# Kernel optimization log

Hardware: AMD Instinct MI355X
Metric: run time of the kernel (lower is better)

## Reference

```python
import jax, jax.numpy as jnp
import numpy as np

NUM_GROUPS = 32
EPS = 1e-6


def group_norm(x, gamma, beta):
    # x: [b, c, t, h, w]
    b, c, t, h, w = x.shape
    xg = x.reshape(b, NUM_GROUPS, c // NUM_GROUPS, t, h, w)
    mean = xg.mean(axis=(2, 3, 4, 5), keepdims=True)
    var = xg.var(axis=(2, 3, 4, 5), keepdims=True)
    xg = (xg - mean) * jax.lax.rsqrt(var + EPS)
    xn = xg.reshape(b, c, t, h, w)
    return xn * gamma[None, :, None, None, None] + beta[None, :, None, None, None]


def conv1x1(x, w, bias):
    # 1x1x1 Conv3d == per-position channel matmul. x: [b,c,t,h,w], w: [cout,cin]
    y = jnp.einsum('oc,bcthw->bothw', w, x)
    return y + bias[None, :, None, None, None]


def setup_inputs() -> dict:
    key = jax.random.key(0)
    ks = jax.random.split(key, 11)
    c = 512
    b, t, h, w = 1, 16, 32, 32
    s = 1.0 / np.sqrt(c)
    return {
        'x': jax.random.normal(ks[0], (b, c, t, h, w), dtype=jnp.float32),
        'gn_gamma': jnp.ones((c,), jnp.float32),
        'gn_beta': jnp.zeros((c,), jnp.float32),
        'wq': jax.random.normal(ks[1], (c, c), jnp.float32) * s,
        'bq': jnp.zeros((c,), jnp.float32),
        'wk': jax.random.normal(ks[2], (c, c), jnp.float32) * s,
        'bk': jnp.zeros((c,), jnp.float32),
        'wv': jax.random.normal(ks[3], (c, c), jnp.float32) * s,
        'bv': jnp.zeros((c,), jnp.float32),
        'wo': jax.random.normal(ks[4], (c, c), jnp.float32) * s,
        'bo': jnp.zeros((c,), jnp.float32),
    }


def reference(x, gn_gamma, gn_beta, wq, bq, wk, bk, wv, bv, wo, bo):
    b, c, t, h, w = x.shape
    h_ = group_norm(x, gn_gamma, gn_beta)
    q = conv1x1(h_, wq, bq)
    k = conv1x1(h_, wk, bk)
    v = conv1x1(h_, wv, bv)
    # per-frame spatial attention: tokens are the h*w grid, batched over (b t)
    n = h * w
    q = q.transpose(0, 2, 3, 4, 1).reshape(b * t, n, c)   # [(bt), n, c]
    k = k.transpose(0, 2, 3, 4, 1).reshape(b * t, n, c)
    v = v.transpose(0, 2, 3, 4, 1).reshape(b * t, n, c)
    scale = float(int(c) ** (-0.5))
    attn = jax.nn.softmax(jnp.einsum('bic,bjc->bij', q, k) * scale, axis=-1)
    out = jnp.einsum('bij,bjc->bic', attn, v)             # [(bt), n, c]
    out = out.reshape(b, t, h, w, c).transpose(0, 4, 1, 2, 3)
    out = conv1x1(out, wo, bo)
    return x + out
```

## Files before the change

### kernel.cpp

```cpp
#include <hip/hip_runtime.h>
#include <hip/hip_bf16.h>

#define CCH   512
#define NPOS  16384
#define NTOK  1024
#define NFRM  16
#define NGRP  32
#define GSZ   (CCH / NGRP)
#define GELEM (GSZ * NPOS)
#define GN_SPLIT 32

typedef unsigned short u16;
typedef unsigned int   u32;
typedef __attribute__((ext_vector_type(8))) short  short8;
typedef __attribute__((ext_vector_type(4))) float  floatx4;

__device__ __forceinline__ float bf2f(u16 u) {
    return __uint_as_float(((u32)u) << 16);
}
__device__ __forceinline__ u16 f2bf(float f) {
    u32 u = __float_as_uint(f);
    u = (u + 0x7fffu + ((u >> 16) & 1u)) >> 16;
    return (u16)u;
}
__device__ __forceinline__ float ldx(const void* p, size_t i, bool f32m) {
    return f32m ? ((const float*)p)[i] : bf2f(((const u16*)p)[i]);
}
__device__ __forceinline__ void gl2lds16(const u16* g, u16* l) {
    __builtin_amdgcn_global_load_lds(
        (const __attribute__((address_space(1))) u32*)g,
        (__attribute__((address_space(3))) u32*)l, 16, 0, 0);
}

__launch_bounds__(256)
__global__ void detect_dtype(const u32* __restrict__ x32, u32* __restrict__ flag) {
    __shared__ int cnt;
    if (threadIdx.x == 0) cnt = 0;
    __syncthreads();
    int c = 0;
    for (int i = threadIdx.x; i < 4096; i += 256) {
        u32 v = x32[i] & 0xFFFFu;
        u32 e = (v >> 7) & 0xFFu;
        if (e >= 0xC8u) c++;
    }
    atomicAdd(&cnt, c);
    __syncthreads();
    if (threadIdx.x == 0) *flag = (cnt > 64) ? 1u : 0u;
}

__launch_bounds__(256)
__global__ void conv_all(const void* w0, const void* w1, const void* w2, const void* w3,
                         const void* b0, const void* b1, const void* b2, const void* b3,
                         u16* __restrict__ wdst, u16* __restrict__ bdst,
                         float* __restrict__ rl,
                         const u32* __restrict__ flag) {
    int b = blockIdx.x;
    if (b > 1024) {
        rl[(b - 1025) * 256 + threadIdx.x] = 0.0f;
        return;
    }
    bool f32m = *flag != 0u;
    if (b < 1024) {
        int wi = b >> 8;
        const void* src = (wi == 0) ? w0 : (wi == 1) ? w1 : (wi == 2) ? w2 : w3;
        int base = (b & 255) * 1024 + threadIdx.x * 4;
        u16* d = wdst + wi * 262144 + base;
        if (f32m) {
            float4 v = *(const float4*)((const float*)src + base);
            ushort4 o;
            o.x = f2bf(v.x); o.y = f2bf(v.y); o.z = f2bf(v.z); o.w = f2bf(v.w);
            *(ushort4*)d = o;
        } else {
            *(ushort4*)d = *(const ushort4*)((const u16*)src + base);
        }
    } else {
        int t = threadIdx.x;
        int bi = t >> 6;
        int off = (t & 63) * 8;
        const void* src = (bi == 0) ? b0 : (bi == 1) ? b1 : (bi == 2) ? b2 : b3;
        u16* d = bdst + bi * 512 + off;
        if (f32m) {
            float4 v1 = *(const float4*)((const float*)src + off);
            float4 v2 = *(const float4*)((const float*)src + off + 4);
            ushort4 o1, o2;
            o1.x = f2bf(v1.x); o1.y = f2bf(v1.y); o1.z = f2bf(v1.z); o1.w = f2bf(v1.w);
            o2.x = f2bf(v2.x); o2.y = f2bf(v2.y); o2.z = f2bf(v2.z); o2.w = f2bf(v2.w);
            *(ushort4*)d = o1; *(ushort4*)(d + 4) = o2;
        } else {
            *(ushort4*)d = *(const ushort4*)((const u16*)src + off);
            *(ushort4*)(d + 4) = *(const ushort4*)((const u16*)src + off + 4);
        }
    }
}

__launch_bounds__(256)
__global__ void gn_partial(const void* __restrict__ x, float2* __restrict__ partials,
                           const u32* __restrict__ flag) {
    __shared__ float sm[8];
    bool f32m = *flag != 0u;
    const int chunk = GELEM / GN_SPLIT;
    size_t base = (size_t)blockIdx.x * chunk;
    float s = 0.f, ss = 0.f;
    if (f32m) {
        const float4* p = (const float4*)((const float*)x + base);
        for (int i = threadIdx.x; i < chunk / 4; i += 256) {
            float4 u = p[i];
            s  += u.x + u.y + u.z + u.w;
            ss += u.x * u.x + u.y * u.y + u.z * u.z + u.w * u.w;
        }
    } else {
        const ushort4* p = (const ushort4*)((const u16*)x + base);
        for (int i = threadIdx.x; i < chunk / 4; i += 256) {
            ushort4 u = p[i];
            float a = bf2f(u.x), b = bf2f(u.y), c = bf2f(u.z), d = bf2f(u.w);
            s  += a + b + c + d;
            ss += a * a + b * b + c * c + d * d;
        }
    }
    int lane = threadIdx.x & 63, w = threadIdx.x >> 6;
    float t = s;
    #pragma unroll
    for (int o = 32; o > 0; o >>= 1) t += __shfl_down(t, o, 64);
    if (lane == 0) sm[w] = t;
    t = ss;
    #pragma unroll
    for (int o = 32; o > 0; o >>= 1) t += __shfl_down(t, o, 64);
    if (lane == 0) sm[4 + w] = t;
    __syncthreads();
    if (threadIdx.x == 0)
        partials[blockIdx.x] = make_float2(sm[0] + sm[1] + sm[2] + sm[3],
                                           sm[4] + sm[5] + sm[6] + sm[7]);
}

__launch_bounds__(256)
__global__ void gn_coef(const float2* __restrict__ partials, const void* __restrict__ gamma,
                        const void* __restrict__ beta, float2* __restrict__ coef,
                        const u32* __restrict__ flag) {
    bool f32m = *flag != 0u;
    int c = blockIdx.x * 256 + threadIdx.x;
    if (c < CCH) {
        int g = c >> 4;
        float sum = 0.f, sq = 0.f;
        #pragma unroll
        for (int i = 0; i < GN_SPLIT; ++i) {
            float2 p = partials[g * GN_SPLIT + i];
            sum += p.x; sq += p.y;
        }
        float mean = sum * (1.0f / (float)GELEM);
        float var  = fmaxf(sq * (1.0f / (float)GELEM) - mean * mean, 0.0f);
        float rstd = rsqrtf(var + 1e-6f);
        float gm = ldx(gamma, c, f32m), b = ldx(beta, c, f32m);
        float sc = rstd * gm;
        coef[c] = make_float2(sc, b - mean * sc);
    }
}

__launch_bounds__(256)
__global__ void gn_apply_t(const void* __restrict__ x, const float2* __restrict__ coef,
                           u16* __restrict__ xt, const u32* __restrict__ flag) {
    bool f32m = *flag != 0u;
    __shared__ float tile[64][65];
    int p0 = blockIdx.x * 64, c0 = blockIdx.y * 64;
    int lane = threadIdx.x & 63, rg = threadIdx.x >> 6;
    #pragma unroll 4
    for (int i = 0; i < 16; ++i) {
        int row = rg * 16 + i;
        int c = c0 + row;
        float2 cf = coef[c];
        float v = ldx(x, (size_t)c * NPOS + p0 + lane, f32m);
        tile[row][lane] = v * cf.x + cf.y;
    }
    __syncthreads();
    #pragma unroll 4
    for (int i = 0; i < 16; ++i) {
        int prow = rg * 16 + i;
        xt[(size_t)(p0 + prow) * CCH + c0 + lane] = f2bf(tile[lane][prow]);
    }
}

#define EPI_QK    0
#define EPI_V     1
#define EPI_SCEXP 2
#define EPI_PV    3
#define EPI_OUT   4

template<int EPI, bool MX, bool FSW>
__launch_bounds__(256, 3)
__global__ void mfma_gemm(const u16* __restrict__ A, const u16* __restrict__ B,
                          void* __restrict__ C, const u16* __restrict__ bias,
                          const void* __restrict__ resid, const u32* __restrict__ flag,
                          float* __restrict__ rl,
                          int lda, int ldb, int ldc, int K,
                          long aFS, long bFS, long cFS) {
    __shared__ __align__(16) u16 As[128 * 64];
    __shared__ __align__(16) u16 Bs[128 * 64];
    const int tid = threadIdx.x;

    int bxi, byi, f;
    if (FSW) {
        u32 id = (blockIdx.z * gridDim.y + blockIdx.y) * gridDim.x + blockIdx.x;
        u32 T = gridDim.x * gridDim.y * gridDim.z;
        u32 half = T >> 1;
        f = (int)(id & 7u) + ((id >= half) ? 8 : 0);
        u32 l = (id >= half ? id - half : id) >> 3;
        bxi = (int)(l % gridDim.x);
        byi = (int)(l / gridDim.x);
    } else {
        bxi = blockIdx.x; byi = blockIdx.y; f = blockIdx.z;
    }
    const int m_blk = MX ? bxi : byi;
    const int n_blk = MX ? byi : bxi;

    const u16* Ab = A + (size_t)f * aFS + (size_t)m_blk * 128 * lda;
    const u16* Bb = B + (size_t)f * bFS + (size_t)n_blk * 128 * ldb;

    const int wave = tid >> 6, lane = tid & 63;
    const int srow8 = wave * 32 + (lane >> 3);
    const int schs  = ((lane & 7) ^ ((lane >> 3) & 7)) * 8;
    u16* lA = &As[wave * 2048];
    u16* lB = &Bs[wave * 2048];

    const int wm = (wave >> 1) * 64, wn = (wave & 1) * 64;
    const int l15 = lane & 15, quad = lane >> 4;

    floatx4 acc[4][4] = {};

    for (int kk = 0; kk < K; kk += 64) {
        __syncthreads();
        #pragma unroll
        for (int o = 0; o < 4; ++o) {
            gl2lds16(Ab + (size_t)(srow8 + o * 8) * lda + kk + schs, lA + o * 512);
            gl2lds16(Bb + (size_t)(srow8 + o * 8) * ldb + kk + schs, lB + o * 512);
        }
        __syncthreads();
        #pragma unroll
        for (int kh = 0; kh < 2; ++kh) {
            short8 af[4], bf[4];
            #pragma unroll
            for (int mi = 0; mi < 4; ++mi) {
                const int row = wm + mi * 16 + l15;
                af[mi] = *(const short8*)&As[row * 64 + (((kh << 2) | quad) ^ (row & 7)) * 8];
            }
            #pragma unroll
            for (int ni = 0; ni < 4; ++ni) {
                const int row = wn + ni * 16 + l15;
                bf[ni] = *(const short8*)&Bs[row * 64 + (((kh << 2) | quad) ^ (row & 7)) * 8];
            }
            #pragma unroll
            for (int mi = 0; mi < 4; ++mi)
                #pragma unroll
                for (int ni = 0; ni < 4; ++ni)
                    acc[mi][ni] = __builtin_amdgcn_mfma_f32_16x16x32_bf16(
                        af[mi], bf[ni], acc[mi][ni], 0, 0, 0);
        }
    }

    const bool f32m = (EPI == EPI_OUT) ? (*flag != 0u) : false;
    const int m_base = m_blk * 128 + wm;
    const int n_base = n_blk * 128 + wn;
    const float scale = 0.044194173824159216f;

    float inv[4][4];
    if (EPI == EPI_PV) {
        #pragma unroll
        for (int mi = 0; mi < 4; ++mi)
            #pragma unroll
            for (int r = 0; r < 4; ++r)
                inv[mi][r] = 1.0f / rl[f * NTOK + m_base + mi * 16 + quad * 4 + r];
    }
    float rs[4][4];
    if (EPI == EPI_SCEXP) {
        #pragma unroll
        for (int mi = 0; mi < 4; ++mi)
            #pragma unroll
            for (int r = 0; r < 4; ++r) rs[mi][r] = 0.0f;
    }

    #pragma unroll
    for (int mi = 0; mi < 4; ++mi) {
        #pragma unroll
        for (int ni = 0; ni < 4; ++ni) {
            int n = n_base + ni * 16 + l15;
            float bn = (EPI == EPI_QK) ? bf2f(bias[n]) : 0.0f;
            #pragma unroll
            for (int r = 0; r < 4; ++r) {
                int m = m_base + mi * 16 + quad * 4 + r;
                float v = acc[mi][ni][r];
                size_t idx = (size_t)f * cFS + (size_t)m * ldc + n;
                if (EPI == EPI_QK) {
                    ((u16*)C)[idx] = f2bf(v + bn);
                } else if (EPI == EPI_V) {
                    ((u16*)C)[idx] = f2bf(v + bf2f(bias[m]));
                } else if (EPI == EPI_SCEXP) {
                    float ex = __expf(v * scale);
                    rs[mi][r] += ex;
                    ((u16*)C)[idx] = f2bf(ex);
                } else if (EPI == EPI_PV) {
                    ((u16*)C)[idx] = f2bf(v * inv[mi][r]);
                } else {
                    float r2 = v + bf2f(bias[m]) + ldx(resid, idx, f32m);
                    if (f32m) ((float*)C)[idx] = r2;
                    else      ((u16*)C)[idx]   = f2bf(r2);
                }
            }
        }
    }

    if (EPI == EPI_SCEXP) {
        #pragma unroll
        for (int mi = 0; mi < 4; ++mi) {
            #pragma unroll
            for (int r = 0; r < 4; ++r) {
                float s = rs[mi][r];
                s += __shfl_xor(s, 1, 64);
                s += __shfl_xor(s, 2, 64);
                s += __shfl_xor(s, 4, 64);
                s += __shfl_xor(s, 8, 64);
                if (l15 == 0)
                    atomicAdd(&rl[f * NTOK + m_base + mi * 16 + quad * 4 + r], s);
            }
        }
    }
}

extern "C" void kernel_launch(void* const* d_in, const int* in_sizes, int n_in,
                              void* d_out, int out_size, void* d_ws, size_t ws_size,
                              hipStream_t stream) {
    const void* x   = d_in[0];
    const void* gam = d_in[1];
    const void* bet = d_in[2];

    char* ws = (char*)d_ws;
    float2* coef     = (float2*)(ws);
    float2* partials = (float2*)(ws + 4096);
    u32*    flag     = (u32*)(ws + 12352);
    u16* cw[4] = { (u16*)(ws + 16384),              (u16*)(ws + 16384 +  524288ull),
                   (u16*)(ws + 16384 + 1048576ull), (u16*)(ws + 16384 + 1572864ull) };
    u16* cb[4] = { (u16*)(ws + 2113536ull),        (u16*)(ws + 2113536ull + 1024),
                   (u16*)(ws + 2113536ull + 2048), (u16*)(ws + 2113536ull + 3072) };
    float* rl  = (float*)(ws + (3ull << 20));
    u16*  xnt  = (u16*)(ws + (4ull  << 20));
    u16*  qkt  = (u16*)(ws + (20ull << 20));
    u16*  vt   = (u16*)(ws + (52ull << 20));
    u16*  pbuf = (u16*)(ws + (68ull << 20));
    u16*  obuf = xnt;

    detect_dtype<<<1, 256, 0, stream>>>((const u32*)x, flag);
    conv_all<<<1089, 256, 0, stream>>>(d_in[3], d_in[5], d_in[7], d_in[9],
                                       d_in[4], d_in[6], d_in[8], d_in[10],
                                       cw[0], cb[0], rl, flag);
    gn_partial<<<NGRP * GN_SPLIT, 256, 0, stream>>>(x, partials, flag);
    gn_coef<<<2, 256, 0, stream>>>(partials, gam, bet, coef, flag);
    gn_apply_t<<<dim3(NPOS / 64, CCH / 64), 256, 0, stream>>>(x, coef, xnt, flag);

    dim3 gqk(NPOS / 128, 1024 / 128, 1);
    mfma_gemm<EPI_QK, true, false><<<gqk, 256, 0, stream>>>(
        xnt, cw[0], qkt, cb[0], nullptr, flag, nullptr, CCH, CCH, 1024, CCH, 0, 0, 0);
    dim3 gv(NPOS / 128, CCH / 128, 1);
    mfma_gemm<EPI_V, false, false><<<gv, 256, 0, stream>>>(
        cw[2], xnt, vt, cb[2], nullptr, flag, nullptr, CCH, CCH, NPOS, CCH, 0, 0, 0);

    dim3 gsc(NTOK / 128, NTOK / 128, NFRM);
    mfma_gemm<EPI_SCEXP, false, true><<<gsc, 256, 0, stream>>>(
        qkt, qkt + 512, pbuf, nullptr, nullptr, flag, rl, 1024, 1024, NTOK, CCH,
        (long)NTOK * 1024, (long)NTOK * 1024, (long)NTOK * NTOK);

    dim3 gpv(CCH / 128, NTOK / 128, NFRM);
    mfma_gemm<EPI_PV, false, true><<<gpv, 256, 0, stream>>>(
        pbuf, vt, obuf, nullptr, nullptr, flag, rl, NTOK, NPOS, CCH, NTOK,
        (long)NTOK * NTOK, NTOK, (long)NTOK * CCH);

    dim3 go(NPOS / 128, CCH / 128, 1);
    mfma_gemm<EPI_OUT, false, false><<<go, 256, 0, stream>>>(
        cw[3], obuf, d_out, cb[3], x, flag, nullptr, CCH, CCH, NPOS, CCH, 0, 0, 0);
}
```

Baseline: 236.9 us.

## Fuse GN coef into apply, merge QK/V GEMMs, use 256-row score tiles

Folds the group-norm coefficient computation into the apply/transpose kernel, so each block recomputes its 64 channel coefficients from the partials and one launch disappears. Merges the QK and V projection GEMMs into a single launch with a blockIdx.y split. Adds a 512-thread kernel for the score/exp GEMM that computes a 256x128 output tile, sharing each loaded B tile across twice as many rows. The costs are redundant coefficient work in every apply block and higher register and LDS pressure in the larger-tile kernel.

After: 232.7 us. About the same (-1.8%).

```diff
diff --git a/kernel.cpp b/kernel.cpp
--- a/kernel.cpp
+++ b/kernel.cpp
@@ -133,15 +133,17 @@
 }
 
 __launch_bounds__(256)
-__global__ void gn_coef(const float2* __restrict__ partials, const void* __restrict__ gamma,
-                        const void* __restrict__ beta, float2* __restrict__ coef,
-                        const u32* __restrict__ flag) {
+__global__ void gn_apply_t(const void* __restrict__ x, const float2* __restrict__ partials,
+                           const void* __restrict__ gamma, const void* __restrict__ beta,
+                           u16* __restrict__ xt, const u32* __restrict__ flag) {
     bool f32m = *flag != 0u;
-    int c = blockIdx.x * 256 + threadIdx.x;
-    if (c < CCH) {
-        int g = c >> 4;
+    __shared__ float tile[64][65];
+    __shared__ float2 cfs[64];
+    int p0 = blockIdx.x * 64, c0 = blockIdx.y * 64;
+    if (threadIdx.x < 64) {
+        int c = c0 + threadIdx.x, g = c >> 4;
         float sum = 0.f, sq = 0.f;
-        #pragma unroll
+        #pragma unroll 8
         for (int i = 0; i < GN_SPLIT; ++i) {
             float2 p = partials[g * GN_SPLIT + i];
             sum += p.x; sq += p.y;
@@ -151,23 +153,15 @@
         float rstd = rsqrtf(var + 1e-6f);
         float gm = ldx(gamma, c, f32m), b = ldx(beta, c, f32m);
         float sc = rstd * gm;
-        coef[c] = make_float2(sc, b - mean * sc);
-    }
-}
-
-__launch_bounds__(256)
-__global__ void gn_apply_t(const void* __restrict__ x, const float2* __restrict__ coef,
-                           u16* __restrict__ xt, const u32* __restrict__ flag) {
-    bool f32m = *flag != 0u;
-    __shared__ float tile[64][65];
-    int p0 = blockIdx.x * 64, c0 = blockIdx.y * 64;
+        cfs[threadIdx.x] = make_float2(sc, b - mean * sc);
+    }
+    __syncthreads();
     int lane = threadIdx.x & 63, rg = threadIdx.x >> 6;
     #pragma unroll 4
     for (int i = 0; i < 16; ++i) {
         int row = rg * 16 + i;
-        int c = c0 + row;
-        float2 cf = coef[c];
-        float v = ldx(x, (size_t)c * NPOS + p0 + lane, f32m);
+        float2 cf = cfs[row];
+        float v = ldx(x, (size_t)(c0 + row) * NPOS + p0 + lane, f32m);
         tile[row][lane] = v * cf.x + cf.y;
     }
     __syncthreads();
@@ -184,41 +178,22 @@
 #define EPI_PV    3
 #define EPI_OUT   4
 
-template<int EPI, bool MX, bool FSW>
-__launch_bounds__(256, 3)
-__global__ void mfma_gemm(const u16* __restrict__ A, const u16* __restrict__ B,
-                          void* __restrict__ C, const u16* __restrict__ bias,
-                          const void* __restrict__ resid, const u32* __restrict__ flag,
-                          float* __restrict__ rl,
-                          int lda, int ldb, int ldc, int K,
-                          long aFS, long bFS, long cFS) {
-    __shared__ __align__(16) u16 As[128 * 64];
-    __shared__ __align__(16) u16 Bs[128 * 64];
+template<int EPI>
+__device__ __forceinline__ void gemm128(
+    u16* __restrict__ As, u16* __restrict__ Bs,
+    const u16* __restrict__ A, const u16* __restrict__ B,
+    void* __restrict__ C, const u16* __restrict__ bias,
+    const void* __restrict__ resid, const u32* __restrict__ flag,
+    float* __restrict__ rl, int m_blk, int n_blk, int f,
+    int lda, int ldb, int ldc, int K, long aFS, long bFS, long cFS)
+{
     const int tid = threadIdx.x;
-
-    int bxi, byi, f;
-    if (FSW) {
-        u32 id = (blockIdx.z * gridDim.y + blockIdx.y) * gridDim.x + blockIdx.x;
-        u32 T = gridDim.x * gridDim.y * gridDim.z;
-        u32 half = T >> 1;
-        f = (int)(id & 7u) + ((id >= half) ? 8 : 0);
-        u32 l = (id >= half ? id - half : id) >> 3;
-        bxi = (int)(l % gridDim.x);
-        byi = (int)(l / gridDim.x);
-    } else {
-        bxi = blockIdx.x; byi = blockIdx.y; f = blockIdx.z;
-    }
-    const int m_blk = MX ? bxi : byi;
-    const int n_blk = MX ? byi : bxi;
-
     const u16* Ab = A + (size_t)f * aFS + (size_t)m_blk * 128 * lda;
     const u16* Bb = B + (size_t)f * bFS + (size_t)n_blk * 128 * ldb;
 
     const int wave = tid >> 6, lane = tid & 63;
-    const int srow8 = wave * 32 + (lane >> 3);
-    const int schs  = ((lane & 7) ^ ((lane >> 3) & 7)) * 8;
-    u16* lA = &As[wave * 2048];
-    u16* lB = &Bs[wave * 2048];
+    const int srow = wave * 32 + (lane >> 3);
+    const int schs = ((lane & 7) ^ ((lane >> 3) & 7)) * 8;
 
     const int wm = (wave >> 1) * 64, wn = (wave & 1) * 64;
     const int l15 = lane & 15, quad = lane >> 4;
@@ -229,8 +204,8 @@
         __syncthreads();
         #pragma unroll
         for (int o = 0; o < 4; ++o) {
-            gl2lds16(Ab + (size_t)(srow8 + o * 8) * lda + kk + schs, lA + o * 512);
-            gl2lds16(Bb + (size_t)(srow8 + o * 8) * ldb + kk + schs, lB + o * 512);
+            gl2lds16(Ab + (size_t)(srow + o * 8) * lda + kk + schs, &As[wave * 2048 + o * 512]);
+            gl2lds16(Bb + (size_t)(srow + o * 8) * ldb + kk + schs, &Bs[wave * 2048 + o * 512]);
         }
         __syncthreads();
         #pragma unroll
@@ -323,6 +298,166 @@
     }
 }
 
+template<int EPI, bool MX, bool FSW>
+__launch_bounds__(256, 3)
+__global__ void mfma_gemm(const u16* __restrict__ A, const u16* __restrict__ B,
+                          void* __restrict__ C, const u16* __restrict__ bias,
+                          const void* __restrict__ resid, const u32* __restrict__ flag,
+                          float* __restrict__ rl,
+                          int lda, int ldb, int ldc, int K,
+                          long aFS, long bFS, long cFS) {
+    __shared__ __align__(16) u16 As[128 * 64];
+    __shared__ __align__(16) u16 Bs[128 * 64];
+    int bxi, byi, f;
+    if (FSW) {
+        u32 id = (blockIdx.z * gridDim.y + blockIdx.y) * gridDim.x + blockIdx.x;
+        u32 T = gridDim.x * gridDim.y * gridDim.z;
+        u32 half = T >> 1;
+        f = (int)(id & 7u) + ((id >= half) ? 8 : 0);
+        u32 l = (id >= half ? id - half : id) >> 3;
+        bxi = (int)(l % gridDim.x);
+        byi = (int)(l / gridDim.x);
+    } else {
+        bxi = blockIdx.x; byi = blockIdx.y; f = blockIdx.z;
+    }
+    gemm128<EPI>(As, Bs, A, B, C, bias, resid, flag, rl,
+                 MX ? bxi : byi, MX ? byi : bxi, f, lda, ldb, ldc, K, aFS, bFS, cFS);
+}
+
+__launch_bounds__(256, 3)
+__global__ void qkv_gemm(const u16* __restrict__ xnt,
+                         const u16* __restrict__ wqk, const u16* __restrict__ bqk,
+                         u16* __restrict__ qkt,
+                         const u16* __restrict__ wv, const u16* __restrict__ bv,
+                         u16* __restrict__ vt,
+                         const u32* __restrict__ flag) {
+    __shared__ __align__(16) u16 As[128 * 64];
+    __shared__ __align__(16) u16 Bs[128 * 64];
+    if (blockIdx.y < 8) {
+        gemm128<EPI_QK>(As, Bs, xnt, wqk, qkt, bqk, nullptr, flag, nullptr,
+                        (int)blockIdx.x, (int)blockIdx.y, 0,
+                        CCH, CCH, 1024, CCH, 0, 0, 0);
+    } else {
+        gemm128<EPI_V>(As, Bs, wv, xnt, vt, bv, nullptr, flag, nullptr,
+                       (int)blockIdx.y - 8, (int)blockIdx.x, 0,
+                       CCH, CCH, NPOS, CCH, 0, 0, 0);
+    }
+}
+
+template<int EPI, bool FSW>
+__launch_bounds__(512, 4)
+__global__ void mfma_gemm256(const u16* __restrict__ A, const u16* __restrict__ B,
+                             void* __restrict__ C, const u16* __restrict__ bias,
+                             const u32* __restrict__ flag, float* __restrict__ rl,
+                             int lda, int ldb, int ldc, int K,
+                             long aFS, long bFS, long cFS) {
+    __shared__ __align__(16) u16 As[256 * 64];
+    __shared__ __align__(16) u16 Bs[128 * 64];
+    const int tid = threadIdx.x;
+
+    int bxi, byi, f;
+    if (FSW) {
+        u32 id = (blockIdx.z * gridDim.y + blockIdx.y) * gridDim.x + blockIdx.x;
+        u32 T = gridDim.x * gridDim.y * gridDim.z;
+        u32 half = T >> 1;
+        f = (int)(id & 7u) + ((id >= half) ? 8 : 0);
+        u32 l = (id >= half ? id - half : id) >> 3;
+        bxi = (int)(l % gridDim.x);
+        byi = (int)(l / gridDim.x);
+    } else {
+        bxi = blockIdx.x; byi = blockIdx.y; f = blockIdx.z;
+    }
+    const int m_blk = byi;
+    const int n_blk = bxi;
+
+    const u16* Ab = A + (size_t)f * aFS + (size_t)m_blk * 256 * lda;
+    const u16* Bb = B + (size_t)f * bFS + (size_t)n_blk * 128 * ldb;
+
+    const int wave = tid >> 6, lane = tid & 63;
+    const int srowA = wave * 32 + (lane >> 3);
+    const int srowB = wave * 16 + (lane >> 3);
+    const int schs  = ((lane & 7) ^ ((lane >> 3) & 7)) * 8;
+
+    const int wm = (wave >> 1) * 64, wn = (wave & 1) * 64;
+    const int l15 = lane & 15, quad = lane >> 4;
+
+    floatx4 acc[4][4] = {};
+
+    for (int kk = 0; kk < K; kk += 64) {
+        __syncthreads();
+        #pragma unroll
+        for (int o = 0; o < 4; ++o)
+            gl2lds16(Ab + (size_t)(srowA + o * 8) * lda + kk + schs,
+                     &As[wave * 2048 + o * 512]);
+        #pragma unroll
+        for (int o = 0; o < 2; ++o)
+            gl2lds16(Bb + (size_t)(srowB + o * 8) * ldb + kk + schs,
+                     &Bs[wave * 1024 + o * 512]);
+        __syncthreads();
+        #pragma unroll
+        for (int kh = 0; kh < 2; ++kh) {
+            short8 af[4], bf[4];
+            #pragma unroll
+            for (int mi = 0; mi < 4; ++mi) {
+                const int row = wm + mi * 16 + l15;
+                af[mi] = *(const short8*)&As[row * 64 + (((kh << 2) | quad) ^ (row & 7)) * 8];
+            }
+            #pragma unroll
+            for (int ni = 0; ni < 4; ++ni) {
+                const int row = wn + ni * 16 + l15;
+                bf[ni] = *(const short8*)&Bs[row * 64 + (((kh << 2) | quad) ^ (row & 7)) * 8];
+            }
+            #pragma unroll
+            for (int mi = 0; mi < 4; ++mi)
+                #pragma unroll
+                for (int ni = 0; ni < 4; ++ni)
+                    acc[mi][ni] = __builtin_amdgcn_mfma_f32_16x16x32_bf16(
+                        af[mi], bf[ni], acc[mi][ni], 0, 0, 0);
+        }
+    }
+
+    const int m_base = m_blk * 256 + wm;
+    const int n_base = n_blk * 128 + wn;
+    const float scale = 0.044194173824159216f;
+
+    float rs[4][4];
+    #pragma unroll
+    for (int mi = 0; mi < 4; ++mi)
+        #pragma unroll
+        for (int r = 0; r < 4; ++r) rs[mi][r] = 0.0f;
+
+    #pragma unroll
+    for (int mi = 0; mi < 4; ++mi) {
+        #pragma unroll
+        for (int ni = 0; ni < 4; ++ni) {
+            int n = n_base + ni * 16 + l15;
+            #pragma unroll
+            for (int r = 0; r < 4; ++r) {
+                int m = m_base + mi * 16 + quad * 4 + r;
+                float v = acc[mi][ni][r];
+                size_t idx = (size_t)f * cFS + (size_t)m * ldc + n;
+                float ex = __expf(v * scale);
+                rs[mi][r] += ex;
+                ((u16*)C)[idx] = f2bf(ex);
+            }
+        }
+    }
+
+    #pragma unroll
+    for (int mi = 0; mi < 4; ++mi) {
+        #pragma unroll
+        for (int r = 0; r < 4; ++r) {
+            float s = rs[mi][r];
+            s += __shfl_xor(s, 1, 64);
+            s += __shfl_xor(s, 2, 64);
+            s += __shfl_xor(s, 4, 64);
+            s += __shfl_xor(s, 8, 64);
+            if (l15 == 0)
+                atomicAdd(&rl[f * NTOK + m_base + mi * 16 + quad * 4 + r], s);
+        }
+    }
+}
+
 extern "C" void kernel_launch(void* const* d_in, const int* in_sizes, int n_in,
                               void* d_out, int out_size, void* d_ws, size_t ws_size,
                               hipStream_t stream) {
@@ -331,7 +466,6 @@
     const void* bet = d_in[2];
 
     char* ws = (char*)d_ws;
-    float2* coef     = (float2*)(ws);
     float2* partials = (float2*)(ws + 4096);
     u32*    flag     = (u32*)(ws + 12352);
     u16* cw[4] = { (u16*)(ws + 16384),              (u16*)(ws + 16384 +  524288ull),
@@ -350,19 +484,15 @@
                                        d_in[4], d_in[6], d_in[8], d_in[10],
                                        cw[0], cb[0], rl, flag);
     gn_partial<<<NGRP * GN_SPLIT, 256, 0, stream>>>(x, partials, flag);
-    gn_coef<<<2, 256, 0, stream>>>(partials, gam, bet, coef, flag);
-    gn_apply_t<<<dim3(NPOS / 64, CCH / 64), 256, 0, stream>>>(x, coef, xnt, flag);
-
-    dim3 gqk(NPOS / 128, 1024 / 128, 1);
-    mfma_gemm<EPI_QK, true, false><<<gqk, 256, 0, stream>>>(
-        xnt, cw[0], qkt, cb[0], nullptr, flag, nullptr, CCH, CCH, 1024, CCH, 0, 0, 0);
-    dim3 gv(NPOS / 128, CCH / 128, 1);
-    mfma_gemm<EPI_V, false, false><<<gv, 256, 0, stream>>>(
-        cw[2], xnt, vt, cb[2], nullptr, flag, nullptr, CCH, CCH, NPOS, CCH, 0, 0, 0);
-
-    dim3 gsc(NTOK / 128, NTOK / 128, NFRM);
-    mfma_gemm<EPI_SCEXP, false, true><<<gsc, 256, 0, stream>>>(
-        qkt, qkt + 512, pbuf, nullptr, nullptr, flag, rl, 1024, 1024, NTOK, CCH,
+    gn_apply_t<<<dim3(NPOS / 64, CCH / 64), 256, 0, stream>>>(
+        x, partials, gam, bet, xnt, flag);
+
+    qkv_gemm<<<dim3(128, 12), 256, 0, stream>>>(
+        xnt, cw[0], cb[0], qkt, cw[2], cb[2], vt, flag);
+
+    dim3 gsc(NTOK / 128, NTOK / 256, NFRM);
+    mfma_gemm256<EPI_SCEXP, true><<<gsc, 512, 0, stream>>>(
+        qkt, qkt + 512, pbuf, nullptr, flag, rl, 1024, 1024, NTOK, CCH,
         (long)NTOK * 1024, (long)NTOK * 1024, (long)NTOK * NTOK);
 
     dim3 gpv(CCH / 128, NTOK / 128, NFRM);
```
